# Optimization experiments

Measured on AMD Instinct MI355X. Metric: run time of the kernel, lower is better.

Reference implementation:

```python
import jax, jax.numpy as jnp
import numpy as np

B, N, E = 4, 4096, 65536
HID, F_N, F_E, ROUNDS = 128, 32, 16, 3


def setup_inputs() -> dict:
    key = jax.random.key(0)
    ks = jax.random.split(key, 32)
    p = lambda k, shape: 0.02 * jax.random.normal(k, shape, dtype=jnp.float32)
    inp = {
        "nodes": jax.random.normal(ks[0], (B, N, F_N), dtype=jnp.float32),
        "edge_feat": jax.random.normal(ks[1], (B, E, F_E), dtype=jnp.float32),
        "edges": jax.random.randint(ks[2], (B, E, 2), 0, N).astype(jnp.int64),
        "node_mask": jnp.ones((B, N), dtype=bool),
        "edge_mask": jnp.ones((B, E), dtype=bool),
        # projections (stored as (in, out))
        "W_node": p(ks[3], (F_N, HID)),
        "W_edge": p(ks[4], (F_E, HID)),
        "marker": p(ks[5], (HID,)),
        # per-round MLP weights, stacked on leading rounds dim
        "eW1": p(ks[6], (ROUNDS, 3 * HID, HID)),
        "eb1": jnp.zeros((ROUNDS, HID), jnp.float32),
        "eW2": p(ks[7], (ROUNDS, HID, HID)),
        "eb2": jnp.zeros((ROUNDS, HID), jnp.float32),
        "nW1": p(ks[8], (ROUNDS, 2 * HID, HID)),
        "nb1": jnp.zeros((ROUNDS, HID), jnp.float32),
        "nW2": p(ks[9], (ROUNDS, HID, HID)),
        "nb2": jnp.zeros((ROUNDS, HID), jnp.float32),
    }
    return inp


def reference(nodes, edge_feat, edges, node_mask, edge_mask,
              W_node, W_edge, marker, eW1, eb1, eW2, eb2, nW1, nb1, nW2, nb2):
    b, n, _ = nodes.shape
    h = nodes @ W_node                       # (B,N,H)
    ef = edge_feat @ W_edge                  # (B,E,H)
    src = jnp.clip(edges[..., 0], 0, n - 1)  # (B,E)
    dst = jnp.clip(edges[..., 1], 0, n - 1)
    bidx = jnp.arange(b)[:, None]            # (B,1) for batched gather/scatter
    em = edge_mask.astype(h.dtype)[..., None]
    nm = node_mask.astype(h.dtype)[..., None]
    for r in range(ROUNDS):
        h_src = h[bidx, src]                 # (B,E,H) gather
        h_dst = h[bidx, dst]
        cat = jnp.concatenate([h_src, h_dst, ef], axis=-1)   # (B,E,3H)
        msg = jax.nn.silu(cat @ eW1[r] + eb1[r]) @ eW2[r] + eb2[r]
        msg = msg * em
        agg = jnp.zeros_like(h).at[bidx, dst].add(msg)       # scatter-add to nodes
        cat_node = jnp.concatenate([h, agg], axis=-1)        # (B,N,2H)
        upd = jax.nn.silu(cat_node @ nW1[r] + nb1[r]) @ nW2[r] + nb2[r]
        h = (h + upd) * nm
    marker_tok = jnp.broadcast_to(marker[None, None, :], (b, 1, HID))
    return jnp.concatenate([marker_tok, h], axis=1)          # (B,1+N,H)
```

## Files before the change

kernel.cpp:

```cpp
#include <hip/hip_runtime.h>
#include <hip/hip_bf16.h>
#include <cstdint>
#include <cstddef>

#define BB 4
#define NN 4096
#define EE 65536
#define HID 128
#define FN 32
#define FE 16
#define NROUNDS 3

#define XP 168
#define XNP 264
#define PP 136
#define YPITCH 136

typedef __attribute__((ext_vector_type(8))) short short8;
typedef __attribute__((ext_vector_type(4))) float f32x4;
typedef unsigned int uint_t;

__device__ __forceinline__ size_t hrow(int b, int n) {
    return ((size_t)b * (NN + 1) + 1 + n) * HID;
}

__device__ __forceinline__ short f2bf(float f) {
    __hip_bfloat16 h = __float2bfloat16(f);
    return *reinterpret_cast<short*>(&h);
}

__device__ __forceinline__ float bf2f(short s) {
    union { uint32_t u; float f; } v;
    v.u = ((uint32_t)(unsigned short)s) << 16;
    return v.f;
}

__device__ __forceinline__ float silu(float x) {
    return x * __builtin_amdgcn_rcpf(1.0f + __expf(-x));
}

__device__ __forceinline__ int clipn(int x) {
    return x < 0 ? 0 : (x > NN - 1 ? NN - 1 : x);
}

__global__ void proj_nodes_kernel(const float* __restrict__ nodes,
                                  const float* __restrict__ Wn,
                                  float* __restrict__ hbuf,
                                  short* __restrict__ hbf,
                                  const float* __restrict__ marker,
                                  const float* __restrict__ We,
                                  const float* __restrict__ eW1,
                                  float* __restrict__ Wec,
                                  uint_t* __restrict__ cnt) {
    __shared__ float nd[8][FN];
    int t = threadIdx.x;
    int row0 = blockIdx.x * 8;

    if (blockIdx.x < 4) {
        hbuf[((size_t)blockIdx.x * (NN + 1)) * HID + t] = marker[t];
    } else if (blockIdx.x < 68) {
        int base = (blockIdx.x - 4) * 256 + t * 2;
        cnt[base] = 0u; cnt[base + 1] = 0u;
    } else if (blockIdx.x < 116) {
        int lb = blockIdx.x - 68; int r = lb >> 4; int i = lb & 15;
        const float* w1 = eW1 + ((size_t)r * 384 + 256) * HID;
        float acc = 0.f;
        for (int k = 0; k < HID; ++k)
            acc += We[i * HID + k] * w1[k * HID + t];
        Wec[((size_t)r * 16 + i) * HID + t] = acc;
    }

    for (int i = 0; i < 2; ++i) {
        int idx = i * 128 + t; int r = idx >> 5; int c = idx & 31;
        nd[r][c] = nodes[(size_t)(row0 + r) * FN + c];
    }
    __syncthreads();
    float acc[8] = {0.f,0.f,0.f,0.f,0.f,0.f,0.f,0.f};
    #pragma unroll
    for (int k = 0; k < FN; ++k) {
        float w = Wn[k * HID + t];
        #pragma unroll
        for (int r = 0; r < 8; ++r) acc[r] += nd[r][k] * w;
    }
    #pragma unroll
    for (int r = 0; r < 8; ++r) {
        int row = row0 + r; int b = row >> 12; int n = row & (NN - 1);
        hbuf[hrow(b, n) + t] = acc[r];
        hbf[(size_t)row * HID + t] = f2bf(acc[r]);
    }
}

__device__ __forceinline__ void pack_generic(const float* __restrict__ W,
                                             short* __restrict__ P,
                                             int KT, size_t rstrideW,
                                             int lb, int lane) {
    int nt = lb & 7;
    int kt = (lb >> 3) % KT;
    int r  = lb / (8 * KT);
    const float* Wr = W + (size_t)r * rstrideW;
    int n  = nt * 16 + (lane & 15);
    int k0 = kt * 32 + (lane >> 4) * 8;
    short v[8];
    #pragma unroll
    for (int i = 0; i < 8; ++i) v[i] = f2bf(Wr[(size_t)(k0 + i) * HID + n]);
    size_t idx = (((size_t)(r * KT + kt) * 8 + nt) * 64 + lane) * 8;
    *(uint4*)&P[idx] = *(uint4*)v;
}

__global__ void pack_all_kernel(const float* __restrict__ eW1,
                                const float* __restrict__ Wec,
                                const float* __restrict__ eW2,
                                const float* __restrict__ nW1,
                                const float* __restrict__ nW2,
                                short* __restrict__ W1p,
                                short* __restrict__ W2p,
                                short* __restrict__ eYp,
                                short* __restrict__ nW1p,
                                short* __restrict__ nW2p) {
    int lane = threadIdx.x;
    int bid = blockIdx.x;
    if (bid < 120) {
        const int KT = 5;
        int nt = bid & 7; int kt = (bid >> 3) % KT; int r = bid / (8 * KT);
        int n  = nt * 16 + (lane & 15);
        int k0 = kt * 32 + (lane >> 4) * 8;
        short v[8];
        #pragma unroll
        for (int i = 0; i < 8; ++i) {
            int k = k0 + i;
            float x;
            if (k < 128)      x = eW1[((size_t)r * 384 + k) * HID + n];
            else if (k < 144) x = Wec[((size_t)r * 16 + (k - 128)) * HID + n];
            else              x = 0.f;
            v[i] = f2bf(x);
        }
        size_t idx = (((size_t)(r * KT + kt) * 8 + nt) * 64 + lane) * 8;
        *(uint4*)&W1p[idx] = *(uint4*)v;
    } else if (bid < 216) {
        pack_generic(eW2, W2p, 4, (size_t)HID * HID, bid - 120, lane);
    } else if (bid < 312) {
        pack_generic(eW1 + (size_t)128 * HID, eYp, 4, (size_t)384 * HID,
                     bid - 216, lane);
    } else if (bid < 504) {
        pack_generic(nW1, nW1p, 8, (size_t)2 * HID * HID, bid - 312, lane);
    } else {
        pack_generic(nW2, nW2p, 4, (size_t)HID * HID, bid - 504, lane);
    }
}

__global__ void hist_kernel(const int* __restrict__ edges,
                            uint_t* __restrict__ cnt) {
    int i = blockIdx.x * 256 + threadIdx.x;
    int b = i >> 16;
    int2 pr = *(const int2*)&edges[(size_t)i * 2];
    int d = clipn(pr.y);
    atomicAdd(&cnt[b * NN + d], 1u);
}

__global__ void scan_kernel(const uint_t* __restrict__ cnt,
                            uint_t* __restrict__ cursor) {
    __shared__ uint_t ps[256];
    int t = threadIdx.x;
    const uint4* c4 = (const uint4*)cnt + (size_t)t * 16;
    uint4 v[16];
    uint_t s = 0;
    #pragma unroll
    for (int i = 0; i < 16; ++i) {
        v[i] = c4[i];
        s += v[i].x + v[i].y + v[i].z + v[i].w;
    }
    ps[t] = s;
    __syncthreads();
    for (int off = 1; off < 256; off <<= 1) {
        uint_t x = (t >= off) ? ps[t - off] : 0u;
        __syncthreads();
        ps[t] += x;
        __syncthreads();
    }
    uint_t run = ps[t] - s;
    uint4* o4 = (uint4*)cursor + (size_t)t * 16;
    #pragma unroll
    for (int i = 0; i < 16; ++i) {
        uint4 o;
        o.x = run;
        o.y = o.x + v[i].x;
        o.z = o.y + v[i].y;
        o.w = o.z + v[i].z;
        run = o.w + v[i].w;
        o4[i] = o;
    }
}

__global__ void scatter_permute_kernel(const int* __restrict__ edges,
                                       const int* __restrict__ emask,
                                       const float* __restrict__ edge_feat,
                                       uint_t* __restrict__ cursor,
                                       uint_t* __restrict__ meta,
                                       short* __restrict__ efs) {
    int i = blockIdx.x * 256 + threadIdx.x;
    int b = i >> 16;
    int2 pr = *(const int2*)&edges[(size_t)i * 2];
    int s = clipn(pr.x), d = clipn(pr.y);
    uint_t mk = emask[i] ? 1u : 0u;
    uint_t p = atomicAdd(&cursor[b * NN + d], 1u);
    meta[p] = (uint_t)s | ((uint_t)d << 12) | (mk << 24);
    const float* src = edge_feat + (size_t)i * FE;
    short v[16];
    #pragma unroll
    for (int k = 0; k < 16; ++k) v[k] = f2bf(src[k]);
    *(uint4*)(efs + (size_t)p * FE)     = *(uint4*)v;
    *(uint4*)(efs + (size_t)p * FE + 8) = *(uint4*)(v + 8);
}

__global__ __launch_bounds__(256, 6)
void proj_y_kernel(const short* __restrict__ hbf,
                   const short* __restrict__ Wp,
                   const float* __restrict__ b1,
                   short* __restrict__ Y,
                   float* __restrict__ agg) {
    __shared__ short X[16 * YPITCH];
    int t = threadIdx.x;
    int row0 = blockIdx.x * 16;

    #pragma unroll
    for (int i = 0; i < 2; ++i) {
        int c = i * 256 + t;
        *(float4*)(agg + (size_t)row0 * HID + c * 4) =
            make_float4(0.f, 0.f, 0.f, 0.f);
    }
    {
        int e = t >> 4; int s = t & 15;
        uint4 v = *(const uint4*)(hbf + (size_t)(row0 + e) * HID + s * 8);
        *(uint4*)((char*)X + e * (YPITCH * 2) + s * 16) = v;
    }
    __syncthreads();

    int lane = t & 63;
    int w    = t >> 6;
    int n0 = w * 32;
    int lr = lane & 15;
    int lg = lane >> 4;

    f32x4 acc[2];
    #pragma unroll
    for (int nf = 0; nf < 2; ++nf) {
        float bv = b1[n0 + nf * 16 + lr];
        acc[nf] = (f32x4){bv, bv, bv, bv};
    }
    const char* Xb = (const char*)X;
    for (int kt = 0; kt < 4; ++kt) {
        short8 a = *(const short8*)(Xb + lr * (YPITCH * 2)
                                       + (kt * 32 + lg * 8) * 2);
        const short* wp = Wp + (((size_t)kt * 8 + (n0 >> 4)) * 64 + lane) * 8;
        #pragma unroll
        for (int nf = 0; nf < 2; ++nf) {
            short8 bf = *(const short8*)(wp + (size_t)nf * 64 * 8);
            acc[nf] = __builtin_amdgcn_mfma_f32_16x16x32_bf16(a, bf, acc[nf], 0, 0, 0);
        }
    }
    #pragma unroll
    for (int r = 0; r < 4; ++r) {
        int row = lg * 4 + r;
        #pragma unroll
        for (int nf = 0; nf < 2; ++nf)
            Y[(size_t)(row0 + row) * HID + n0 + nf * 16 + lr]
                = f2bf(acc[nf][r]);
    }
}

__global__ __launch_bounds__(256, 6)
void edge_mfma_csr_kernel(const short* __restrict__ hbf,
                          const short* __restrict__ efs,
                          const uint_t* __restrict__ meta,
                          const short* __restrict__ Y,
                          const short* __restrict__ W1p,
                          const short* __restrict__ W2p,
                          const float* __restrict__ b2,
                          float* __restrict__ agg) {
    __shared__ short X[64 * XP];
    __shared__ int sdst[64];
    __shared__ float smf[64];
    __shared__ unsigned short segs[65];
    __shared__ int nseg;
    short* Pl = X;

    int t = threadIdx.x;
    int p0 = blockIdx.x * 64;
    int b  = p0 >> 16;

    if (t < 64) {
        uint_t m = meta[p0 + t];
        sdst[t] = (int)((m >> 12) & 0xFFFu);
        smf[t]  = (m >> 24) ? 1.f : 0.f;
        uint_t pm = __shfl_up(m, 1);
        int flag = (t == 0) || (((m ^ pm) & 0x00FFF000u) != 0u);
        unsigned long long mask = __ballot(flag);
        int rank = __popcll(mask & ((1ull << t) - 1ull));
        if (flag) segs[rank] = (unsigned short)t;
        if (t == 0) {
            int ns = __popcll(mask);
            nseg = ns;
            segs[ns] = 64;
        }
    }
    __syncthreads();

    #pragma unroll
    for (int i = 0; i < 4; ++i) {
        int c = i * 256 + t; int e = c >> 4; int s = c & 15;
        int src = (int)(meta[p0 + e] & 0xFFFu);
        uint4 v = *(const uint4*)(hbf + ((size_t)b * NN + src) * HID + s * 8);
        *(uint4*)((char*)X + e * (XP * 2) + s * 16) = v;
    }
    if (t < 128) {
        int e = t >> 1; int s = t & 1;
        uint4 v = *(const uint4*)(efs + (size_t)(p0 + e) * FE + s * 8);
        *(uint4*)((char*)X + e * (XP * 2) + 256 + s * 16) = v;
        *(uint4*)((char*)X + e * (XP * 2) + 288 + s * 16) = make_uint4(0,0,0,0);
    }

    int lane = t & 63;
    int w    = t >> 6;
    int m0 = (w & 1) * 32;
    int n0 = (w >> 1) * 64;
    int lr = lane & 15;
    int lg = lane >> 4;

    f32x4 acc[2][4];
    #pragma unroll
    for (int mf = 0; mf < 2; ++mf)
        #pragma unroll
        for (int r = 0; r < 4; ++r) {
            int row = m0 + mf * 16 + lg * 4 + r;
            const short* yp = Y + ((size_t)b * NN + sdst[row]) * HID + n0 + lr;
            #pragma unroll
            for (int nf = 0; nf < 4; ++nf)
                acc[mf][nf][r] = bf2f(yp[nf * 16]);
        }
    __syncthreads();

    const char* Xb = (const char*)X;
    for (int kt = 0; kt < 5; ++kt) {
        short8 a[2];
        #pragma unroll
        for (int mf = 0; mf < 2; ++mf)
            a[mf] = *(const short8*)(Xb + (m0 + mf * 16 + lr) * (XP * 2)
                                        + (kt * 32 + lg * 8) * 2);
        const short* wp = W1p + (((size_t)kt * 8 + (n0 >> 4)) * 64 + lane) * 8;
        #pragma unroll
        for (int nf = 0; nf < 4; ++nf) {
            short8 bf = *(const short8*)(wp + (size_t)nf * 64 * 8);
            #pragma unroll
            for (int mf = 0; mf < 2; ++mf)
                acc[mf][nf] = __builtin_amdgcn_mfma_f32_16x16x32_bf16(
                    a[mf], bf, acc[mf][nf], 0, 0, 0);
        }
    }
    __syncthreads();

    #pragma unroll
    for (int mf = 0; mf < 2; ++mf)
        #pragma unroll
        for (int nf = 0; nf < 4; ++nf)
            #pragma unroll
            for (int r = 0; r < 4; ++r) {
                int row = m0 + mf * 16 + lg * 4 + r;
                int col = n0 + nf * 16 + lr;
                Pl[row * PP + col] = f2bf(silu(acc[mf][nf][r]));
            }
    __syncthreads();

    f32x4 acc2[2][4];
    #pragma unroll
    for (int nf = 0; nf < 4; ++nf) {
        float bv = b2[n0 + nf * 16 + lr];
        #pragma unroll
        for (int mf = 0; mf < 2; ++mf)
            acc2[mf][nf] = (f32x4){bv, bv, bv, bv};
    }
    const char* Pb = (const char*)Pl;
    for (int kt = 0; kt < 4; ++kt) {
        short8 a[2];
        #pragma unroll
        for (int mf = 0; mf < 2; ++mf)
            a[mf] = *(const short8*)(Pb + (m0 + mf * 16 + lr) * (PP * 2)
                                        + (kt * 32 + lg * 8) * 2);
        const short* wp = W2p + (((size_t)kt * 8 + (n0 >> 4)) * 64 + lane) * 8;
        #pragma unroll
        for (int nf = 0; nf < 4; ++nf) {
            short8 bf = *(const short8*)(wp + (size_t)nf * 64 * 8);
            #pragma unroll
            for (int mf = 0; mf < 2; ++mf)
                acc2[mf][nf] = __builtin_amdgcn_mfma_f32_16x16x32_bf16(
                    a[mf], bf, acc2[mf][nf], 0, 0, 0);
        }
    }
    __syncthreads();

    #pragma unroll
    for (int mf = 0; mf < 2; ++mf)
        #pragma unroll
        for (int r = 0; r < 4; ++r) {
            int row = m0 + mf * 16 + lg * 4 + r;
            float m = smf[row];
            #pragma unroll
            for (int nf = 0; nf < 4; ++nf)
                Pl[row * PP + n0 + nf * 16 + lr] = f2bf(acc2[mf][nf][r] * m);
        }
    __syncthreads();

    {
        int ns = nseg;
        for (int task = t; task < (ns << 7); task += 256) {
            int s = task >> 7;
            int c = task & 127;
            int r0 = segs[s], r1 = segs[s + 1];
            float run = 0.f;
            for (int r = r0; r < r1; ++r)
                run += bf2f(Pl[r * PP + c]);
            atomicAdd(&agg[((size_t)b * NN + sdst[r0]) * HID + c], run);
        }
    }
}

__global__ __launch_bounds__(256, 6)
void node_mfma_kernel(const short* __restrict__ hbf_in,
                      const float* __restrict__ agg,
                      const int* __restrict__ nmask,
                      const short* __restrict__ W1p,
                      const short* __restrict__ W2p,
                      const float* __restrict__ b1,
                      const float* __restrict__ b2,
                      float* __restrict__ hout,
                      short* __restrict__ hbf_out,
                      short* __restrict__ Ynext,
                      const short* __restrict__ eYpN,
                      const float* __restrict__ b1N,
                      float* __restrict__ aggz) {
    __shared__ short X[16 * XNP];
    __shared__ int smk[16];
    short* Pl = X;

    int t = threadIdx.x;
    int row0 = blockIdx.x * 16;
    int b  = row0 >> 12;
    int nn0 = row0 & (NN - 1);

    if (t < 16) smk[t] = nmask[row0 + t];

    {
        int e = t >> 4; int s = t & 15;
        uint4 v = *(const uint4*)(hbf_in + (size_t)(row0 + e) * HID + s * 8);
        *(uint4*)((char*)X + e * (XNP * 2) + s * 16) = v;
    }
    #pragma unroll
    for (int i = 0; i < 2; ++i) {
        int c = i * 256 + t; int e = c >> 5; int s = c & 31;
        float4 f = *(const float4*)(agg + (size_t)(row0 + e) * HID + s * 4);
        short v[4] = { f2bf(f.x), f2bf(f.y), f2bf(f.z), f2bf(f.w) };
        *(uint2*)((char*)X + e * (XNP * 2) + 256 + s * 8) = *(uint2*)v;
    }
    __syncthreads();

    int lane = t & 63;
    int w    = t >> 6;
    int n0 = w * 32;
    int lr = lane & 15;
    int lg = lane >> 4;

    f32x4 acc[2];
    #pragma unroll
    for (int nf = 0; nf < 2; ++nf) {
        float bv = b1[n0 + nf * 16 + lr];
        acc[nf] = (f32x4){bv, bv, bv, bv};
    }
    const char* Xb = (const char*)X;
    for (int kt = 0; kt < 8; ++kt) {
        short8 a = *(const short8*)(Xb + lr * (XNP * 2)
                                       + (kt * 32 + lg * 8) * 2);
        const short* wp = W1p + (((size_t)kt * 8 + (n0 >> 4)) * 64 + lane) * 8;
        #pragma unroll
        for (int nf = 0; nf < 2; ++nf) {
            short8 bf = *(const short8*)(wp + (size_t)nf * 64 * 8);
            acc[nf] = __builtin_amdgcn_mfma_f32_16x16x32_bf16(a, bf, acc[nf], 0, 0, 0);
        }
    }
    __syncthreads();

    #pragma unroll
    for (int nf = 0; nf < 2; ++nf)
        #pragma unroll
        for (int r = 0; r < 4; ++r) {
            int row = lg * 4 + r;
            int col = n0 + nf * 16 + lr;
            Pl[row * PP + col] = f2bf(silu(acc[nf][r]));
        }
    __syncthreads();

    f32x4 acc2[2];
    #pragma unroll
    for (int nf = 0; nf < 2; ++nf) {
        float bv = b2[n0 + nf * 16 + lr];
        acc2[nf] = (f32x4){bv, bv, bv, bv};
    }
    const char* Pb = (const char*)Pl;
    for (int kt = 0; kt < 4; ++kt) {
        short8 a = *(const short8*)(Pb + lr * (PP * 2)
                                       + (kt * 32 + lg * 8) * 2);
        const short* wp = W2p + (((size_t)kt * 8 + (n0 >> 4)) * 64 + lane) * 8;
        #pragma unroll
        for (int nf = 0; nf < 2; ++nf) {
            short8 bf = *(const short8*)(wp + (size_t)nf * 64 * 8);
            acc2[nf] = __builtin_amdgcn_mfma_f32_16x16x32_bf16(a, bf, acc2[nf], 0, 0, 0);
        }
    }

    short hn_bf[2][4];
    #pragma unroll
    for (int r = 0; r < 4; ++r) {
        int rl = lg * 4 + r;
        float m = smk[rl] ? 1.f : 0.f;
        size_t ho = hrow(b, nn0 + rl);
        size_t hb = (size_t)(row0 + rl) * HID;
        #pragma unroll
        for (int nf = 0; nf < 2; ++nf) {
            int col = n0 + nf * 16 + lr;
            float hold = hout[ho + col];
            float hn = (hold + acc2[nf][r]) * m;
            hout[ho + col] = hn;
            short hb16 = f2bf(hn);
            hbf_out[hb + col] = hb16;
            hn_bf[nf][r] = hb16;
        }
    }

    if (Ynext == nullptr) return;

    __syncthreads();
    #pragma unroll
    for (int r = 0; r < 4; ++r) {
        int row = lg * 4 + r;
        #pragma unroll
        for (int nf = 0; nf < 2; ++nf)
            Pl[row * PP + n0 + nf * 16 + lr] = hn_bf[nf][r];
    }
    __syncthreads();

    f32x4 accy[2];
    #pragma unroll
    for (int nf = 0; nf < 2; ++nf) {
        float bv = b1N[n0 + nf * 16 + lr];
        accy[nf] = (f32x4){bv, bv, bv, bv};
    }
    for (int kt = 0; kt < 4; ++kt) {
        short8 a = *(const short8*)((const char*)Pl + lr * (PP * 2)
                                       + (kt * 32 + lg * 8) * 2);
        const short* wp = eYpN + (((size_t)kt * 8 + (n0 >> 4)) * 64 + lane) * 8;
        #pragma unroll
        for (int nf = 0; nf < 2; ++nf) {
            short8 bf = *(const short8*)(wp + (size_t)nf * 64 * 8);
            accy[nf] = __builtin_amdgcn_mfma_f32_16x16x32_bf16(a, bf, accy[nf], 0, 0, 0);
        }
    }
    #pragma unroll
    for (int r = 0; r < 4; ++r) {
        int row = lg * 4 + r;
        #pragma unroll
        for (int nf = 0; nf < 2; ++nf)
            Ynext[(size_t)(row0 + row) * HID + n0 + nf * 16 + lr]
                = f2bf(accy[nf][r]);
    }
    #pragma unroll
    for (int i = 0; i < 2; ++i) {
        int c = i * 256 + t;
        *(float4*)(aggz + (size_t)row0 * HID + c * 4) =
            make_float4(0.f, 0.f, 0.f, 0.f);
    }
}

extern "C" void kernel_launch(void* const* d_in, const int* in_sizes, int n_in,
                              void* d_out, int out_size, void* d_ws, size_t ws_size,
                              hipStream_t stream) {
    const float* nodes     = (const float*)d_in[0];
    const float* edge_feat = (const float*)d_in[1];
    const int*   edges     = (const int*)d_in[2];
    const int*   node_mask = (const int*)d_in[3];
    const int*   edge_mask = (const int*)d_in[4];
    const float* W_node    = (const float*)d_in[5];
    const float* W_edge    = (const float*)d_in[6];
    const float* marker    = (const float*)d_in[7];
    const float* eW1       = (const float*)d_in[8];
    const float* eb1       = (const float*)d_in[9];
    const float* eW2       = (const float*)d_in[10];
    const float* eb2       = (const float*)d_in[11];
    const float* nW1       = (const float*)d_in[12];
    const float* nb1       = (const float*)d_in[13];
    const float* nW2       = (const float*)d_in[14];
    const float* nb2       = (const float*)d_in[15];
    float* out = (float*)d_out;

    const size_t HN = (size_t)BB * NN * HID;
    char* wsb = (char*)d_ws;
    float*  agg    = (float*)wsb;   wsb += HN * 4;
    short*  hbf    = (short*)wsb;   wsb += HN * 2;
    short*  Yb     = (short*)wsb;   wsb += HN * 2;
    float*  Wec    = (float*)wsb;   wsb += 3 * 16 * HID * 4;
    short*  W1p    = (short*)wsb;   wsb += 3 * 5 * 4096 * 2;
    short*  W2p    = (short*)wsb;   wsb += 3 * 4 * 4096 * 2;
    short*  eYp    = (short*)wsb;   wsb += 3 * 4 * 4096 * 2;
    short*  nW1p   = (short*)wsb;   wsb += 3 * 8 * 4096 * 2;
    short*  nW2p   = (short*)wsb;   wsb += 3 * 4 * 4096 * 2;
    uint_t* cnt    = (uint_t*)wsb;  wsb += (size_t)BB * NN * 4;
    uint_t* cursor = (uint_t*)wsb;  wsb += (size_t)BB * NN * 4;
    uint_t* meta   = (uint_t*)wsb;  wsb += (size_t)BB * EE * 4;
    short*  efs    = (short*)wsb;   wsb += (size_t)BB * EE * FE * 2;
    if ((size_t)(wsb - (char*)d_ws) > ws_size) return;

    proj_nodes_kernel<<<(BB * NN) / 8, 128, 0, stream>>>(
        nodes, W_node, out, hbf, marker, W_edge, eW1, Wec, cnt);
    pack_all_kernel<<<600, 64, 0, stream>>>(
        eW1, Wec, eW2, nW1, nW2, W1p, W2p, eYp, nW1p, nW2p);
    hist_kernel<<<(BB * EE) / 256, 256, 0, stream>>>(edges, cnt);
    scan_kernel<<<1, 256, 0, stream>>>(cnt, cursor);
    scatter_permute_kernel<<<(BB * EE) / 256, 256, 0, stream>>>(
        edges, edge_mask, edge_feat, cursor, meta, efs);

    proj_y_kernel<<<(BB * NN) / 16, 256, 0, stream>>>(
        hbf, eYp, eb1, Yb, agg);

    for (int r = 0; r < NROUNDS; ++r) {
        edge_mfma_csr_kernel<<<(BB * EE) / 64, 256, 0, stream>>>(
            hbf, efs, meta, Yb,
            W1p + (size_t)r * 5 * 4096,
            W2p + (size_t)r * 4 * 4096,
            eb2 + r * HID,
            agg);
        bool last = (r == NROUNDS - 1);
        node_mfma_kernel<<<(BB * NN) / 16, 256, 0, stream>>>(
            hbf, agg, node_mask,
            nW1p + (size_t)r * 8 * 4096,
            nW2p + (size_t)r * 4 * 4096,
            nb1 + r * HID,
            nb2 + r * HID,
            out, hbf,
            last ? nullptr : Yb,
            last ? eYp : eYp + (size_t)(r + 1) * 4 * 4096,
            last ? eb1 : eb1 + (size_t)(r + 1) * HID,
            agg);
    }
}
```

Measured before the change: 220.1 us.

## Process two edge tiles per block with register-prefetched second tile gather

Each edge block now handles 128 edges as two 64-edge tiles. The second tile's gathered node rows and edge features are loaded into registers before the first tile is computed, then written to shared memory afterwards, so the gather latency overlaps with the MFMA work. The segment-reduction loop also reads two bf16 values per 32-bit load and issues paired atomics. This halves the grid and adds register pressure (stg/efg held across the first tile's compute), which may reduce occupancy under the launch bounds.

Measured after the change: 378.6 us. 1.72x slower.

```diff
diff --git a/kernel.cpp b/kernel.cpp
--- a/kernel.cpp
+++ b/kernel.cpp
@@ -33,6 +33,13 @@
     union { uint32_t u; float f; } v;
     v.u = ((uint32_t)(unsigned short)s) << 16;
     return v.f;
+}
+
+__device__ __forceinline__ float bflo(uint_t u) {
+    union { uint_t u; float f; } v; v.u = u << 16; return v.f;
+}
+__device__ __forceinline__ float bfhi(uint_t u) {
+    union { uint_t u; float f; } v; v.u = u & 0xFFFF0000u; return v.f;
 }
 
 __device__ __forceinline__ float silu(float x) {
@@ -278,46 +285,35 @@
                           const float* __restrict__ b2,
                           float* __restrict__ agg) {
     __shared__ short X[64 * XP];
-    __shared__ int sdst[64];
-    __shared__ float smf[64];
-    __shared__ unsigned short segs[65];
-    __shared__ int nseg;
+    __shared__ int sdst[2][64];
+    __shared__ float smf[2][64];
+    __shared__ unsigned short segs[2][65];
+    __shared__ int nsegs[2];
     short* Pl = X;
 
     int t = threadIdx.x;
-    int p0 = blockIdx.x * 64;
-    int b  = p0 >> 16;
-
-    if (t < 64) {
-        uint_t m = meta[p0 + t];
-        sdst[t] = (int)((m >> 12) & 0xFFFu);
-        smf[t]  = (m >> 24) ? 1.f : 0.f;
+    int p0 = blockIdx.x * 128;
+    int p1 = p0 + 64;
+    int b0 = p0 >> 16;
+    int b1 = p1 >> 16;
+
+    if (t < 128) {
+        int ti = t >> 6; int l = t & 63;
+        uint_t m = meta[(size_t)p0 + (ti << 6) + l];
+        sdst[ti][l] = (int)((m >> 12) & 0xFFFu);
+        smf[ti][l]  = (m >> 24) ? 1.f : 0.f;
         uint_t pm = __shfl_up(m, 1);
-        int flag = (t == 0) || (((m ^ pm) & 0x00FFF000u) != 0u);
+        int flag = (l == 0) || (((m ^ pm) & 0x00FFF000u) != 0u);
         unsigned long long mask = __ballot(flag);
-        int rank = __popcll(mask & ((1ull << t) - 1ull));
-        if (flag) segs[rank] = (unsigned short)t;
-        if (t == 0) {
+        int rank = __popcll(mask & ((1ull << l) - 1ull));
+        if (flag) segs[ti][rank] = (unsigned short)l;
+        if (l == 0) {
             int ns = __popcll(mask);
-            nseg = ns;
-            segs[ns] = 64;
-        }
-    }
-    __syncthreads();
-
-    #pragma unroll
-    for (int i = 0; i < 4; ++i) {
-        int c = i * 256 + t; int e = c >> 4; int s = c & 15;
-        int src = (int)(meta[p0 + e] & 0xFFFu);
-        uint4 v = *(const uint4*)(hbf + ((size_t)b * NN + src) * HID + s * 8);
-        *(uint4*)((char*)X + e * (XP * 2) + s * 16) = v;
-    }
-    if (t < 128) {
-        int e = t >> 1; int s = t & 1;
-        uint4 v = *(const uint4*)(efs + (size_t)(p0 + e) * FE + s * 8);
-        *(uint4*)((char*)X + e * (XP * 2) + 256 + s * 16) = v;
-        *(uint4*)((char*)X + e * (XP * 2) + 288 + s * 16) = make_uint4(0,0,0,0);
-    }
+            nsegs[ti] = ns;
+            segs[ti][ns] = 64;
+        }
+    }
+    __syncthreads();
 
     int lane = t & 63;
     int w    = t >> 6;
@@ -326,101 +322,151 @@
     int lr = lane & 15;
     int lg = lane >> 4;
 
-    f32x4 acc[2][4];
-    #pragma unroll
-    for (int mf = 0; mf < 2; ++mf)
-        #pragma unroll
-        for (int r = 0; r < 4; ++r) {
-            int row = m0 + mf * 16 + lg * 4 + r;
-            const short* yp = Y + ((size_t)b * NN + sdst[row]) * HID + n0 + lr;
-            #pragma unroll
-            for (int nf = 0; nf < 4; ++nf)
-                acc[mf][nf][r] = bf2f(yp[nf * 16]);
-        }
-    __syncthreads();
-
-    const char* Xb = (const char*)X;
-    for (int kt = 0; kt < 5; ++kt) {
-        short8 a[2];
+    #pragma unroll
+    for (int i = 0; i < 4; ++i) {
+        int c = i * 256 + t; int e = c >> 4; int s = c & 15;
+        int src = (int)(meta[(size_t)p0 + e] & 0xFFFu);
+        uint4 v = *(const uint4*)(hbf + ((size_t)b0 * NN + src) * HID + s * 8);
+        *(uint4*)((char*)X + e * (XP * 2) + s * 16) = v;
+    }
+    if (t < 128) {
+        int e = t >> 1; int s = t & 1;
+        uint4 v = *(const uint4*)(efs + (size_t)(p0 + e) * FE + s * 8);
+        *(uint4*)((char*)X + e * (XP * 2) + 256 + s * 16) = v;
+        *(uint4*)((char*)X + e * (XP * 2) + 288 + s * 16) = make_uint4(0,0,0,0);
+    }
+
+    uint4 stg[4];
+    uint4 efg;
+    #pragma unroll
+    for (int i = 0; i < 4; ++i) {
+        int c = i * 256 + t; int e = c >> 4; int s = c & 15;
+        int src = (int)(meta[(size_t)p1 + e] & 0xFFFu);
+        stg[i] = *(const uint4*)(hbf + ((size_t)b1 * NN + src) * HID + s * 8);
+    }
+    if (t < 128) {
+        int e = t >> 1; int s = t & 1;
+        efg = *(const uint4*)(efs + (size_t)(p1 + e) * FE + s * 8);
+    }
+
+    auto compute_tile = [&](int ti, int bb) {
+        f32x4 acc[2][4];
         #pragma unroll
         for (int mf = 0; mf < 2; ++mf)
-            a[mf] = *(const short8*)(Xb + (m0 + mf * 16 + lr) * (XP * 2)
-                                        + (kt * 32 + lg * 8) * 2);
-        const short* wp = W1p + (((size_t)kt * 8 + (n0 >> 4)) * 64 + lane) * 8;
-        #pragma unroll
-        for (int nf = 0; nf < 4; ++nf) {
-            short8 bf = *(const short8*)(wp + (size_t)nf * 64 * 8);
-            #pragma unroll
-            for (int mf = 0; mf < 2; ++mf)
-                acc[mf][nf] = __builtin_amdgcn_mfma_f32_16x16x32_bf16(
-                    a[mf], bf, acc[mf][nf], 0, 0, 0);
-        }
-    }
-    __syncthreads();
-
-    #pragma unroll
-    for (int mf = 0; mf < 2; ++mf)
-        #pragma unroll
-        for (int nf = 0; nf < 4; ++nf)
             #pragma unroll
             for (int r = 0; r < 4; ++r) {
                 int row = m0 + mf * 16 + lg * 4 + r;
-                int col = n0 + nf * 16 + lr;
-                Pl[row * PP + col] = f2bf(silu(acc[mf][nf][r]));
+                const short* yp = Y + ((size_t)bb * NN + sdst[ti][row]) * HID
+                                    + n0 + lr;
+                #pragma unroll
+                for (int nf = 0; nf < 4; ++nf)
+                    acc[mf][nf][r] = bf2f(yp[nf * 16]);
             }
-    __syncthreads();
-
-    f32x4 acc2[2][4];
-    #pragma unroll
-    for (int nf = 0; nf < 4; ++nf) {
-        float bv = b2[n0 + nf * 16 + lr];
+        __syncthreads();
+
+        const char* Xb = (const char*)X;
+        for (int kt = 0; kt < 5; ++kt) {
+            short8 a[2];
+            #pragma unroll
+            for (int mf = 0; mf < 2; ++mf)
+                a[mf] = *(const short8*)(Xb + (m0 + mf * 16 + lr) * (XP * 2)
+                                            + (kt * 32 + lg * 8) * 2);
+            const short* wp = W1p + (((size_t)kt * 8 + (n0 >> 4)) * 64 + lane) * 8;
+            #pragma unroll
+            for (int nf = 0; nf < 4; ++nf) {
+                short8 bf = *(const short8*)(wp + (size_t)nf * 64 * 8);
+                #pragma unroll
+                for (int mf = 0; mf < 2; ++mf)
+                    acc[mf][nf] = __builtin_amdgcn_mfma_f32_16x16x32_bf16(
+                        a[mf], bf, acc[mf][nf], 0, 0, 0);
+            }
+        }
+        __syncthreads();
+
         #pragma unroll
         for (int mf = 0; mf < 2; ++mf)
-            acc2[mf][nf] = (f32x4){bv, bv, bv, bv};
-    }
-    const char* Pb = (const char*)Pl;
-    for (int kt = 0; kt < 4; ++kt) {
-        short8 a[2];
+            #pragma unroll
+            for (int nf = 0; nf < 4; ++nf)
+                #pragma unroll
+                for (int r = 0; r < 4; ++r) {
+                    int row = m0 + mf * 16 + lg * 4 + r;
+                    int col = n0 + nf * 16 + lr;
+                    Pl[row * PP + col] = f2bf(silu(acc[mf][nf][r]));
+                }
+        __syncthreads();
+
+        f32x4 acc2[2][4];
+        #pragma unroll
+        for (int nf = 0; nf < 4; ++nf) {
+            float bv = b2[n0 + nf * 16 + lr];
+            #pragma unroll
+            for (int mf = 0; mf < 2; ++mf)
+                acc2[mf][nf] = (f32x4){bv, bv, bv, bv};
+        }
+        const char* Pb = (const char*)Pl;
+        for (int kt = 0; kt < 4; ++kt) {
+            short8 a[2];
+            #pragma unroll
+            for (int mf = 0; mf < 2; ++mf)
+                a[mf] = *(const short8*)(Pb + (m0 + mf * 16 + lr) * (PP * 2)
+                                            + (kt * 32 + lg * 8) * 2);
+            const short* wp = W2p + (((size_t)kt * 8 + (n0 >> 4)) * 64 + lane) * 8;
+            #pragma unroll
+            for (int nf = 0; nf < 4; ++nf) {
+                short8 bf = *(const short8*)(wp + (size_t)nf * 64 * 8);
+                #pragma unroll
+                for (int mf = 0; mf < 2; ++mf)
+                    acc2[mf][nf] = __builtin_amdgcn_mfma_f32_16x16x32_bf16(
+                        a[mf], bf, acc2[mf][nf], 0, 0, 0);
+            }
+        }
+        __syncthreads();
+
         #pragma unroll
         for (int mf = 0; mf < 2; ++mf)
-            a[mf] = *(const short8*)(Pb + (m0 + mf * 16 + lr) * (PP * 2)
-                                        + (kt * 32 + lg * 8) * 2);
-        const short* wp = W2p + (((size_t)kt * 8 + (n0 >> 4)) * 64 + lane) * 8;
-        #pragma unroll
-        for (int nf = 0; nf < 4; ++nf) {
-            short8 bf = *(const short8*)(wp + (size_t)nf * 64 * 8);
-            #pragma unroll
-            for (int mf = 0; mf < 2; ++mf)
-                acc2[mf][nf] = __builtin_amdgcn_mfma_f32_16x16x32_bf16(
-                    a[mf], bf, acc2[mf][nf], 0, 0, 0);
-        }
-    }
-    __syncthreads();
-
-    #pragma unroll
-    for (int mf = 0; mf < 2; ++mf)
-        #pragma unroll
-        for (int r = 0; r < 4; ++r) {
-            int row = m0 + mf * 16 + lg * 4 + r;
-            float m = smf[row];
-            #pragma unroll
-            for (int nf = 0; nf < 4; ++nf)
-                Pl[row * PP + n0 + nf * 16 + lr] = f2bf(acc2[mf][nf][r] * m);
-        }
-    __syncthreads();
-
-    {
-        int ns = nseg;
-        for (int task = t; task < (ns << 7); task += 256) {
-            int s = task >> 7;
-            int c = task & 127;
-            int r0 = segs[s], r1 = segs[s + 1];
-            float run = 0.f;
-            for (int r = r0; r < r1; ++r)
-                run += bf2f(Pl[r * PP + c]);
-            atomicAdd(&agg[((size_t)b * NN + sdst[r0]) * HID + c], run);
-        }
-    }
+            #pragma unroll
+            for (int r = 0; r < 4; ++r) {
+                int row = m0 + mf * 16 + lg * 4 + r;
+                float m = smf[ti][row];
+                #pragma unroll
+                for (int nf = 0; nf < 4; ++nf)
+                    Pl[row * PP + n0 + nf * 16 + lr]
+                        = f2bf(acc2[mf][nf][r] * m);
+            }
+        __syncthreads();
+
+        int ns = nsegs[ti];
+        for (int task = t; task < (ns << 6); task += 256) {
+            int s  = task >> 6;
+            int c2 = (task & 63) * 2;
+            int r0 = segs[ti][s], r1 = segs[ti][s + 1];
+            float run0 = 0.f, run1 = 0.f;
+            for (int r = r0; r < r1; ++r) {
+                uint_t pr = *(const uint_t*)&Pl[r * PP + c2];
+                run0 += bflo(pr);
+                run1 += bfhi(pr);
+            }
+            float* ap = &agg[((size_t)bb * NN + sdst[ti][r0]) * HID + c2];
+            atomicAdd(ap,     run0);
+            atomicAdd(ap + 1, run1);
+        }
+    };
+
+    compute_tile(0, b0);
+    __syncthreads();
+
+    #pragma unroll
+    for (int i = 0; i < 4; ++i) {
+        int c = i * 256 + t; int e = c >> 4; int s = c & 15;
+        *(uint4*)((char*)X + e * (XP * 2) + s * 16) = stg[i];
+    }
+    if (t < 128) {
+        int e = t >> 1; int s = t & 1;
+        *(uint4*)((char*)X + e * (XP * 2) + 256 + s * 16) = efg;
+        *(uint4*)((char*)X + e * (XP * 2) + 288 + s * 16) = make_uint4(0,0,0,0);
+    }
+
+    compute_tile(1, b1);
 }
 
 __global__ __launch_bounds__(256, 6)
@@ -629,7 +675,7 @@
         hbf, eYp, eb1, Yb, agg);
 
     for (int r = 0; r < NROUNDS; ++r) {
-        edge_mfma_csr_kernel<<<(BB * EE) / 64, 256, 0, stream>>>(
+        edge_mfma_csr_kernel<<<(BB * EE) / 128, 256, 0, stream>>>(
             hbf, efs, meta, Yb,
             W1p + (size_t)r * 5 * 4096,
             W2p + (size_t)r * 4 * 4096,
```

## Load edge MFMA A-operands directly from global, drop X LDS staging

Applied to the files above, without the earlier changes.

The edge kernel no longer gathers the h_src rows and edge features into an LDS tile before the first GEMM. Each lane now loads its MFMA A fragments straight from global memory through per-row source pointers, which removes the X buffer and two barriers and shrinks LDS use. The segment reduction also processes two bf16 columns per thread with one 32-bit LDS read, and the K loops are unrolled. In exchange, each wave re-reads the gathered rows from global or L2, since the other wave that shares the same rows fetches them separately.

After: 245.9 us. +11.7%, slower.

```diff
diff --git a/kernel.cpp b/kernel.cpp
--- a/kernel.cpp
+++ b/kernel.cpp
@@ -11,7 +11,6 @@
 #define FE 16
 #define NROUNDS 3
 
-#define XP 168
 #define XNP 264
 #define PP 136
 #define YPITCH 136
@@ -33,6 +32,13 @@
     union { uint32_t u; float f; } v;
     v.u = ((uint32_t)(unsigned short)s) << 16;
     return v.f;
+}
+
+__device__ __forceinline__ float bflo(uint_t u) {
+    union { uint_t u; float f; } v; v.u = u << 16; return v.f;
+}
+__device__ __forceinline__ float bfhi(uint_t u) {
+    union { uint_t u; float f; } v; v.u = u & 0xFFFF0000u; return v.f;
 }
 
 __device__ __forceinline__ float silu(float x) {
@@ -277,12 +283,12 @@
                           const short* __restrict__ W2p,
                           const float* __restrict__ b2,
                           float* __restrict__ agg) {
-    __shared__ short X[64 * XP];
+    __shared__ short Pl[64 * PP];
+    __shared__ int ssrc[64];
     __shared__ int sdst[64];
     __shared__ float smf[64];
     __shared__ unsigned short segs[65];
     __shared__ int nseg;
-    short* Pl = X;
 
     int t = threadIdx.x;
     int p0 = blockIdx.x * 64;
@@ -290,6 +296,7 @@
 
     if (t < 64) {
         uint_t m = meta[p0 + t];
+        ssrc[t] = (int)(m & 0xFFFu);
         sdst[t] = (int)((m >> 12) & 0xFFFu);
         smf[t]  = (m >> 24) ? 1.f : 0.f;
         uint_t pm = __shfl_up(m, 1);
@@ -305,20 +312,6 @@
     }
     __syncthreads();
 
-    #pragma unroll
-    for (int i = 0; i < 4; ++i) {
-        int c = i * 256 + t; int e = c >> 4; int s = c & 15;
-        int src = (int)(meta[p0 + e] & 0xFFFu);
-        uint4 v = *(const uint4*)(hbf + ((size_t)b * NN + src) * HID + s * 8);
-        *(uint4*)((char*)X + e * (XP * 2) + s * 16) = v;
-    }
-    if (t < 128) {
-        int e = t >> 1; int s = t & 1;
-        uint4 v = *(const uint4*)(efs + (size_t)(p0 + e) * FE + s * 8);
-        *(uint4*)((char*)X + e * (XP * 2) + 256 + s * 16) = v;
-        *(uint4*)((char*)X + e * (XP * 2) + 288 + s * 16) = make_uint4(0,0,0,0);
-    }
-
     int lane = t & 63;
     int w    = t >> 6;
     int m0 = (w & 1) * 32;
@@ -326,6 +319,16 @@
     int lr = lane & 15;
     int lg = lane >> 4;
 
+    int ra = m0 + lr, rb = m0 + 16 + lr;
+    const short* arow[2] = {
+        hbf + ((size_t)b * NN + ssrc[ra]) * HID,
+        hbf + ((size_t)b * NN + ssrc[rb]) * HID
+    };
+    const short* erow[2] = {
+        efs + (size_t)(p0 + ra) * FE,
+        efs + (size_t)(p0 + rb) * FE
+    };
+
     f32x4 acc[2][4];
     #pragma unroll
     for (int mf = 0; mf < 2; ++mf)
@@ -337,15 +340,24 @@
             for (int nf = 0; nf < 4; ++nf)
                 acc[mf][nf][r] = bf2f(yp[nf * 16]);
         }
-    __syncthreads();
-
-    const char* Xb = (const char*)X;
+
+    #pragma unroll
     for (int kt = 0; kt < 5; ++kt) {
         short8 a[2];
-        #pragma unroll
-        for (int mf = 0; mf < 2; ++mf)
-            a[mf] = *(const short8*)(Xb + (m0 + mf * 16 + lr) * (XP * 2)
-                                        + (kt * 32 + lg * 8) * 2);
+        if (kt < 4) {
+            #pragma unroll
+            for (int mf = 0; mf < 2; ++mf)
+                a[mf] = *(const short8*)(arow[mf] + kt * 32 + lg * 8);
+        } else {
+            short8 z = {0,0,0,0,0,0,0,0};
+            if (lg < 2) {
+                #pragma unroll
+                for (int mf = 0; mf < 2; ++mf)
+                    a[mf] = *(const short8*)(erow[mf] + lg * 8);
+            } else {
+                a[0] = z; a[1] = z;
+            }
+        }
         const short* wp = W1p + (((size_t)kt * 8 + (n0 >> 4)) * 64 + lane) * 8;
         #pragma unroll
         for (int nf = 0; nf < 4; ++nf) {
@@ -356,7 +368,6 @@
                     a[mf], bf, acc[mf][nf], 0, 0, 0);
         }
     }
-    __syncthreads();
 
     #pragma unroll
     for (int mf = 0; mf < 2; ++mf)
@@ -379,6 +390,7 @@
             acc2[mf][nf] = (f32x4){bv, bv, bv, bv};
     }
     const char* Pb = (const char*)Pl;
+    #pragma unroll
     for (int kt = 0; kt < 4; ++kt) {
         short8 a[2];
         #pragma unroll
@@ -411,14 +423,19 @@
 
     {
         int ns = nseg;
-        for (int task = t; task < (ns << 7); task += 256) {
-            int s = task >> 7;
-            int c = task & 127;
+        for (int task = t; task < (ns << 6); task += 256) {
+            int s  = task >> 6;
+            int c2 = (task & 63) * 2;
             int r0 = segs[s], r1 = segs[s + 1];
-            float run = 0.f;
-            for (int r = r0; r < r1; ++r)
-                run += bf2f(Pl[r * PP + c]);
-            atomicAdd(&agg[((size_t)b * NN + sdst[r0]) * HID + c], run);
+            float run0 = 0.f, run1 = 0.f;
+            for (int r = r0; r < r1; ++r) {
+                uint_t pr = *(const uint_t*)&Pl[r * PP + c2];
+                run0 += bflo(pr);
+                run1 += bfhi(pr);
+            }
+            float* ap = &agg[((size_t)b * NN + sdst[r0]) * HID + c2];
+            atomicAdd(ap,     run0);
+            atomicAdd(ap + 1, run1);
         }
     }
 }
```

## Fold edge second-layer matmul into node MLP via linearity of scatter-add

Applied to the files above, without the earlier changes.

The edge kernel no longer runs the second edge GEMM (eW2) per edge. It scatters the masked silu activations directly. Because scatter-add is linear, the node kernel instead applies the precomputed product eW2·nW1[agg part] to the aggregated sum, and the eb2 bias becomes a masked-edge-count times a precomputed vector. This removes an E×128×128 GEMM per round, at the cost of computing the fused weights at setup, a per-node masked-count atomic, and some extra bf16 rounding differences.

New measurement: 223.2 us. No clear change (+1.4%).

```diff
diff --git a/kernel.cpp b/kernel.cpp
--- a/kernel.cpp
+++ b/kernel.cpp
@@ -35,6 +35,13 @@
     return v.f;
 }
 
+__device__ __forceinline__ float bflo(uint_t u) {
+    union { uint_t u; float f; } v; v.u = u << 16; return v.f;
+}
+__device__ __forceinline__ float bfhi(uint_t u) {
+    union { uint_t u; float f; } v; v.u = u & 0xFFFF0000u; return v.f;
+}
+
 __device__ __forceinline__ float silu(float x) {
     return x * __builtin_amdgcn_rcpf(1.0f + __expf(-x));
 }
@@ -50,8 +57,12 @@
                                   const float* __restrict__ marker,
                                   const float* __restrict__ We,
                                   const float* __restrict__ eW1,
+                                  const float* __restrict__ eW2,
+                                  const float* __restrict__ nW1,
                                   float* __restrict__ Wec,
-                                  uint_t* __restrict__ cnt) {
+                                  float* __restrict__ F,
+                                  uint_t* __restrict__ cnt,
+                                  uint_t* __restrict__ cntm) {
     __shared__ float nd[8][FN];
     int t = threadIdx.x;
     int row0 = blockIdx.x * 8;
@@ -60,7 +71,8 @@
         hbuf[((size_t)blockIdx.x * (NN + 1)) * HID + t] = marker[t];
     } else if (blockIdx.x < 68) {
         int base = (blockIdx.x - 4) * 256 + t * 2;
-        cnt[base] = 0u; cnt[base + 1] = 0u;
+        cnt[base] = 0u;  cnt[base + 1] = 0u;
+        cntm[base] = 0u; cntm[base + 1] = 0u;
     } else if (blockIdx.x < 116) {
         int lb = blockIdx.x - 68; int r = lb >> 4; int i = lb & 15;
         const float* w1 = eW1 + ((size_t)r * 384 + 256) * HID;
@@ -68,6 +80,14 @@
         for (int k = 0; k < HID; ++k)
             acc += We[i * HID + k] * w1[k * HID + t];
         Wec[((size_t)r * 16 + i) * HID + t] = acc;
+    } else if (blockIdx.x < 500) {
+        int lb = blockIdx.x - 116; int r = lb >> 7; int k = lb & 127;
+        const float* w2r = eW2 + ((size_t)r * HID + k) * HID;
+        const float* n1r = nW1 + ((size_t)r * 256 + 128) * HID;
+        float acc = 0.f;
+        for (int j = 0; j < HID; ++j)
+            acc += w2r[j] * n1r[j * HID + t];
+        F[((size_t)r * HID + k) * HID + t] = acc;
     }
 
     for (int i = 0; i < 2; ++i) {
@@ -109,14 +129,15 @@
 
 __global__ void pack_all_kernel(const float* __restrict__ eW1,
                                 const float* __restrict__ Wec,
-                                const float* __restrict__ eW2,
+                                const float* __restrict__ F,
                                 const float* __restrict__ nW1,
                                 const float* __restrict__ nW2,
+                                const float* __restrict__ eb2,
                                 short* __restrict__ W1p,
-                                short* __restrict__ W2p,
                                 short* __restrict__ eYp,
                                 short* __restrict__ nW1p,
-                                short* __restrict__ nW2p) {
+                                short* __restrict__ nW2p,
+                                float* __restrict__ vecb) {
     int lane = threadIdx.x;
     int bid = blockIdx.x;
     if (bid < 120) {
@@ -137,14 +158,35 @@
         size_t idx = (((size_t)(r * KT + kt) * 8 + nt) * 64 + lane) * 8;
         *(uint4*)&W1p[idx] = *(uint4*)v;
     } else if (bid < 216) {
-        pack_generic(eW2, W2p, 4, (size_t)HID * HID, bid - 120, lane);
-    } else if (bid < 312) {
         pack_generic(eW1 + (size_t)128 * HID, eYp, 4, (size_t)384 * HID,
-                     bid - 216, lane);
+                     bid - 120, lane);
+    } else if (bid < 408) {
+        const int KT = 8;
+        int lb = bid - 216;
+        int nt = lb & 7; int kt = (lb >> 3) % KT; int r = lb / (8 * KT);
+        int n  = nt * 16 + (lane & 15);
+        int k0 = kt * 32 + (lane >> 4) * 8;
+        short v[8];
+        #pragma unroll
+        for (int i = 0; i < 8; ++i) {
+            int k = k0 + i;
+            float x;
+            if (k < 128) x = nW1[((size_t)r * 256 + k) * HID + n];
+            else         x = F[((size_t)r * HID + (k - 128)) * HID + n];
+            v[i] = f2bf(x);
+        }
+        size_t idx = (((size_t)(r * KT + kt) * 8 + nt) * 64 + lane) * 8;
+        *(uint4*)&nW1p[idx] = *(uint4*)v;
     } else if (bid < 504) {
-        pack_generic(nW1, nW1p, 8, (size_t)2 * HID * HID, bid - 312, lane);
+        pack_generic(nW2, nW2p, 4, (size_t)HID * HID, bid - 408, lane);
     } else {
-        pack_generic(nW2, nW2p, 4, (size_t)HID * HID, bid - 504, lane);
+        int idx = (bid - 504) * 64 + lane;
+        int r = idx >> 7; int col = idx & 127;
+        const float* n1r = nW1 + ((size_t)r * 256 + 128) * HID;
+        float acc = 0.f;
+        for (int j = 0; j < HID; ++j)
+            acc += eb2[r * HID + j] * n1r[j * HID + col];
+        vecb[r * HID + col] = acc;
     }
 }
 
@@ -196,12 +238,14 @@
                                        const float* __restrict__ edge_feat,
                                        uint_t* __restrict__ cursor,
                                        uint_t* __restrict__ meta,
-                                       short* __restrict__ efs) {
+                                       short* __restrict__ efs,
+                                       uint_t* __restrict__ cntm) {
     int i = blockIdx.x * 256 + threadIdx.x;
     int b = i >> 16;
     int2 pr = *(const int2*)&edges[(size_t)i * 2];
     int s = clipn(pr.x), d = clipn(pr.y);
     uint_t mk = emask[i] ? 1u : 0u;
+    if (mk) atomicAdd(&cntm[b * NN + d], 1u);
     uint_t p = atomicAdd(&cursor[b * NN + d], 1u);
     meta[p] = (uint_t)s | ((uint_t)d << 12) | (mk << 24);
     const float* src = edge_feat + (size_t)i * FE;
@@ -217,7 +261,7 @@
                    const short* __restrict__ Wp,
                    const float* __restrict__ b1,
                    short* __restrict__ Y,
-                   float* __restrict__ agg) {
+                   float* __restrict__ S) {
     __shared__ short X[16 * YPITCH];
     int t = threadIdx.x;
     int row0 = blockIdx.x * 16;
@@ -225,7 +269,7 @@
     #pragma unroll
     for (int i = 0; i < 2; ++i) {
         int c = i * 256 + t;
-        *(float4*)(agg + (size_t)row0 * HID + c * 4) =
+        *(float4*)(S + (size_t)row0 * HID + c * 4) =
             make_float4(0.f, 0.f, 0.f, 0.f);
     }
     {
@@ -274,9 +318,7 @@
                           const uint_t* __restrict__ meta,
                           const short* __restrict__ Y,
                           const short* __restrict__ W1p,
-                          const short* __restrict__ W2p,
-                          const float* __restrict__ b2,
-                          float* __restrict__ agg) {
+                          float* __restrict__ S) {
     __shared__ short X[64 * XP];
     __shared__ int sdst[64];
     __shared__ float smf[64];
@@ -366,66 +408,34 @@
             for (int r = 0; r < 4; ++r) {
                 int row = m0 + mf * 16 + lg * 4 + r;
                 int col = n0 + nf * 16 + lr;
-                Pl[row * PP + col] = f2bf(silu(acc[mf][nf][r]));
+                Pl[row * PP + col] = f2bf(smf[row] * silu(acc[mf][nf][r]));
             }
-    __syncthreads();
-
-    f32x4 acc2[2][4];
-    #pragma unroll
-    for (int nf = 0; nf < 4; ++nf) {
-        float bv = b2[n0 + nf * 16 + lr];
-        #pragma unroll
-        for (int mf = 0; mf < 2; ++mf)
-            acc2[mf][nf] = (f32x4){bv, bv, bv, bv};
-    }
-    const char* Pb = (const char*)Pl;
-    for (int kt = 0; kt < 4; ++kt) {
-        short8 a[2];
-        #pragma unroll
-        for (int mf = 0; mf < 2; ++mf)
-            a[mf] = *(const short8*)(Pb + (m0 + mf * 16 + lr) * (PP * 2)
-                                        + (kt * 32 + lg * 8) * 2);
-        const short* wp = W2p + (((size_t)kt * 8 + (n0 >> 4)) * 64 + lane) * 8;
-        #pragma unroll
-        for (int nf = 0; nf < 4; ++nf) {
-            short8 bf = *(const short8*)(wp + (size_t)nf * 64 * 8);
-            #pragma unroll
-            for (int mf = 0; mf < 2; ++mf)
-                acc2[mf][nf] = __builtin_amdgcn_mfma_f32_16x16x32_bf16(
-                    a[mf], bf, acc2[mf][nf], 0, 0, 0);
-        }
-    }
-    __syncthreads();
-
-    #pragma unroll
-    for (int mf = 0; mf < 2; ++mf)
-        #pragma unroll
-        for (int r = 0; r < 4; ++r) {
-            int row = m0 + mf * 16 + lg * 4 + r;
-            float m = smf[row];
-            #pragma unroll
-            for (int nf = 0; nf < 4; ++nf)
-                Pl[row * PP + n0 + nf * 16 + lr] = f2bf(acc2[mf][nf][r] * m);
-        }
     __syncthreads();
 
     {
         int ns = nseg;
-        for (int task = t; task < (ns << 7); task += 256) {
-            int s = task >> 7;
-            int c = task & 127;
+        for (int task = t; task < (ns << 6); task += 256) {
+            int s  = task >> 6;
+            int c2 = (task & 63) * 2;
             int r0 = segs[s], r1 = segs[s + 1];
-            float run = 0.f;
-            for (int r = r0; r < r1; ++r)
-                run += bf2f(Pl[r * PP + c]);
-            atomicAdd(&agg[((size_t)b * NN + sdst[r0]) * HID + c], run);
+            float run0 = 0.f, run1 = 0.f;
+            for (int r = r0; r < r1; ++r) {
+                uint_t pr = *(const uint_t*)&Pl[r * PP + c2];
+                run0 += bflo(pr);
+                run1 += bfhi(pr);
+            }
+            float* ap = &S[((size_t)b * NN + sdst[r0]) * HID + c2];
+            atomicAdd(ap,     run0);
+            atomicAdd(ap + 1, run1);
         }
     }
 }
 
 __global__ __launch_bounds__(256, 6)
 void node_mfma_kernel(const short* __restrict__ hbf_in,
-                      const float* __restrict__ agg,
+                      const float* __restrict__ S,
+                      const uint_t* __restrict__ cntm,
+                      const float* __restrict__ vec,
                       const int* __restrict__ nmask,
                       const short* __restrict__ W1p,
                       const short* __restrict__ W2p,
@@ -436,9 +446,10 @@
                       short* __restrict__ Ynext,
                       const short* __restrict__ eYpN,
                       const float* __restrict__ b1N,
-                      float* __restrict__ aggz) {
+                      float* __restrict__ Sz) {
     __shared__ short X[16 * XNP];
     __shared__ int smk[16];
+    __shared__ float scnt[16];
     short* Pl = X;
 
     int t = threadIdx.x;
@@ -446,7 +457,10 @@
     int b  = row0 >> 12;
     int nn0 = row0 & (NN - 1);
 
-    if (t < 16) smk[t] = nmask[row0 + t];
+    if (t < 16) {
+        smk[t]  = nmask[row0 + t];
+        scnt[t] = (float)cntm[row0 + t];
+    }
 
     {
         int e = t >> 4; int s = t & 15;
@@ -456,7 +470,7 @@
     #pragma unroll
     for (int i = 0; i < 2; ++i) {
         int c = i * 256 + t; int e = c >> 5; int s = c & 31;
-        float4 f = *(const float4*)(agg + (size_t)(row0 + e) * HID + s * 4);
+        float4 f = *(const float4*)(S + (size_t)(row0 + e) * HID + s * 4);
         short v[4] = { f2bf(f.x), f2bf(f.y), f2bf(f.z), f2bf(f.w) };
         *(uint2*)((char*)X + e * (XNP * 2) + 256 + s * 8) = *(uint2*)v;
     }
@@ -471,8 +485,12 @@
     f32x4 acc[2];
     #pragma unroll
     for (int nf = 0; nf < 2; ++nf) {
-        float bv = b1[n0 + nf * 16 + lr];
-        acc[nf] = (f32x4){bv, bv, bv, bv};
+        int col = n0 + nf * 16 + lr;
+        float bv = b1[col];
+        float vv = vec[col];
+        #pragma unroll
+        for (int r = 0; r < 4; ++r)
+            acc[nf][r] = bv + scnt[lg * 4 + r] * vv;
     }
     const char* Xb = (const char*)X;
     for (int kt = 0; kt < 8; ++kt) {
@@ -573,7 +591,7 @@
     #pragma unroll
     for (int i = 0; i < 2; ++i) {
         int c = i * 256 + t;
-        *(float4*)(aggz + (size_t)row0 * HID + c * 4) =
+        *(float4*)(Sz + (size_t)row0 * HID + c * 4) =
             make_float4(0.f, 0.f, 0.f, 0.f);
     }
 }
@@ -601,43 +619,44 @@
 
     const size_t HN = (size_t)BB * NN * HID;
     char* wsb = (char*)d_ws;
-    float*  agg    = (float*)wsb;   wsb += HN * 4;
+    float*  S      = (float*)wsb;   wsb += HN * 4;
     short*  hbf    = (short*)wsb;   wsb += HN * 2;
     short*  Yb     = (short*)wsb;   wsb += HN * 2;
     float*  Wec    = (float*)wsb;   wsb += 3 * 16 * HID * 4;
+    float*  F      = (float*)wsb;   wsb += 3 * HID * HID * 4;
+    float*  vecb   = (float*)wsb;   wsb += 3 * HID * 4;
     short*  W1p    = (short*)wsb;   wsb += 3 * 5 * 4096 * 2;
-    short*  W2p    = (short*)wsb;   wsb += 3 * 4 * 4096 * 2;
     short*  eYp    = (short*)wsb;   wsb += 3 * 4 * 4096 * 2;
     short*  nW1p   = (short*)wsb;   wsb += 3 * 8 * 4096 * 2;
     short*  nW2p   = (short*)wsb;   wsb += 3 * 4 * 4096 * 2;
     uint_t* cnt    = (uint_t*)wsb;  wsb += (size_t)BB * NN * 4;
     uint_t* cursor = (uint_t*)wsb;  wsb += (size_t)BB * NN * 4;
+    uint_t* cntm   = (uint_t*)wsb;  wsb += (size_t)BB * NN * 4;
     uint_t* meta   = (uint_t*)wsb;  wsb += (size_t)BB * EE * 4;
     short*  efs    = (short*)wsb;   wsb += (size_t)BB * EE * FE * 2;
     if ((size_t)(wsb - (char*)d_ws) > ws_size) return;
 
     proj_nodes_kernel<<<(BB * NN) / 8, 128, 0, stream>>>(
-        nodes, W_node, out, hbf, marker, W_edge, eW1, Wec, cnt);
-    pack_all_kernel<<<600, 64, 0, stream>>>(
-        eW1, Wec, eW2, nW1, nW2, W1p, W2p, eYp, nW1p, nW2p);
+        nodes, W_node, out, hbf, marker, W_edge, eW1, eW2, nW1,
+        Wec, F, cnt, cntm);
+    pack_all_kernel<<<510, 64, 0, stream>>>(
+        eW1, Wec, F, nW1, nW2, eb2, W1p, eYp, nW1p, nW2p, vecb);
     hist_kernel<<<(BB * EE) / 256, 256, 0, stream>>>(edges, cnt);
     scan_kernel<<<1, 256, 0, stream>>>(cnt, cursor);
     scatter_permute_kernel<<<(BB * EE) / 256, 256, 0, stream>>>(
-        edges, edge_mask, edge_feat, cursor, meta, efs);
+        edges, edge_mask, edge_feat, cursor, meta, efs, cntm);
 
     proj_y_kernel<<<(BB * NN) / 16, 256, 0, stream>>>(
-        hbf, eYp, eb1, Yb, agg);
+        hbf, eYp, eb1, Yb, S);
 
     for (int r = 0; r < NROUNDS; ++r) {
         edge_mfma_csr_kernel<<<(BB * EE) / 64, 256, 0, stream>>>(
             hbf, efs, meta, Yb,
             W1p + (size_t)r * 5 * 4096,
-            W2p + (size_t)r * 4 * 4096,
-            eb2 + r * HID,
-            agg);
+            S);
         bool last = (r == NROUNDS - 1);
         node_mfma_kernel<<<(BB * NN) / 16, 256, 0, stream>>>(
-            hbf, agg, node_mask,
+            hbf, S, cntm, vecb + (size_t)r * HID, node_mask,
             nW1p + (size_t)r * 8 * 4096,
             nW2p + (size_t)r * 4 * 4096,
             nb1 + r * HID,
@@ -646,6 +665,6 @@
             last ? nullptr : Yb,
             last ? eYp : eYp + (size_t)(r + 1) * 4 * 4096,
             last ? eb1 : eb1 + (size_t)(r + 1) * HID,
-            agg);
-    }
-}
+            S);
+    }
+}
```
